# Kernel optimization log

Hardware: AMD Instinct MI355X
Metric: run time of the kernel (lower is better)

The kernel has to match this reference:

```python
import jax, jax.numpy as jnp
import numpy as np

N_NODES = 100000
N_EDGES = 800000
N_GRAPHS = 64
D_IN = 128
D_HID = 128
D_OUT = 128
N_VARS = 8


def setup_inputs() -> dict:
    key = jax.random.key(0)
    ks = jax.random.split(key, 12)
    s = 1.0 / np.sqrt(D_IN)
    inp = {
        "features": jax.random.normal(ks[0], (N_NODES, D_IN), jnp.float32),
        "src": jax.random.randint(ks[1], (N_EDGES,), 0, N_NODES, jnp.int32),
        "dst": jax.random.randint(ks[2], (N_EDGES,), 0, N_NODES, jnp.int32),
        "graph_id": jnp.sort(jax.random.randint(ks[3], (N_NODES,), 0, N_GRAPHS, jnp.int32)),
        # GINConv MLP params (Linear + ReLU per layer)
        "W1": jax.random.normal(ks[4], (D_IN, D_HID), jnp.float32) * s,
        "b1": jnp.zeros((D_HID,), jnp.float32),
        "W2": jax.random.normal(ks[5], (D_HID, D_HID), jnp.float32) * s,
        "b2": jnp.zeros((D_HID,), jnp.float32),
        "W3": jax.random.normal(ks[6], (D_HID, D_OUT), jnp.float32) * s,
        "b3": jnp.zeros((D_OUT,), jnp.float32),
        # final prediction head
        "Wp": jax.random.normal(ks[7], (D_OUT, N_VARS), jnp.float32) * s,
        "bp": jnp.zeros((N_VARS,), jnp.float32),
    }
    return inp


def reference(features, src, dst, graph_id, W1, b1, W2, b2, W3, b3, Wp, bp):
    N = features.shape[0]

    def gin_layer(x, W, b):
        # DGL GINConv with eps=0: apply_func(x + sum_{j in N(i)} x_j)
        agg = jax.ops.segment_sum(x[src], dst, num_segments=N)  # [N, d]
        return jax.nn.relu((x + agg) @ W + b)

    h = gin_layer(features, W1, b1)  # dropout p=0 -> identity
    h = gin_layer(h, W2, b2)
    h = gin_layer(h, W3, b3)

    # dgl.mean_nodes: ragged per-graph mean readout
    sums = jax.ops.segment_sum(h, graph_id, num_segments=N_GRAPHS)          # [G, d]
    cnts = jax.ops.segment_sum(jnp.ones((N, 1), h.dtype), graph_id, num_segments=N_GRAPHS)
    pooled = sums / jnp.maximum(cnts, 1.0)
    return pooled @ Wp + bp  # [G, n_vars]
```

## Files before the change

### kernel.cpp

```cpp
#include <hip/hip_runtime.h>
#include <cstddef>

#define NN 100000
#define NE 800000
#define NG 64
#define DD 128
#define NV 8
#define NS 8
#define SCAN_CH 1024
#define SCAN_NB ((NN + SCAN_CH - 1) / SCAN_CH)
#define NPC 256
#define NCHUNK ((NN + NPC - 1) / NPC)

#define CVT_BLKS 6250
#define WT_BLKS 192
#define HCH 392
#define ECH ((NE + HCH - 1) / HCH)
#define RNG 12500

typedef __attribute__((ext_vector_type(8))) short bf16x8;
typedef __attribute__((ext_vector_type(4))) float f32x4;
typedef __attribute__((ext_vector_type(2))) unsigned int u32x2;

__device__ inline float lo2f(unsigned int u) {
  union { unsigned int i; float f; } x;
  x.i = u << 16;
  return x.f;
}
__device__ inline float hi2f(unsigned int u) {
  union { unsigned int i; float f; } x;
  x.i = u & 0xffff0000u;
  return x.f;
}
__device__ inline unsigned short f2b(float f) {
  union { float f; unsigned int i; } x;
  x.f = f;
  unsigned int r = x.i + 0x7fffu + ((x.i >> 16) & 1u);
  return (unsigned short)(r >> 16);
}
__device__ inline unsigned int pk(float a, float b) {
  return (unsigned int)f2b(a) | ((unsigned int)f2b(b) << 16);
}

__global__ __launch_bounds__(256) void zero_w(unsigned int* __restrict__ p, int n) {
  int i = blockIdx.x * blockDim.x + threadIdx.x;
  if (i < n) p[i] = 0u;
}

__global__ __launch_bounds__(256) void prep(const float* __restrict__ feat,
                                            const float* __restrict__ W1,
                                            const float* __restrict__ W2,
                                            const float* __restrict__ W3,
                                            const int* __restrict__ dst,
                                            unsigned short* __restrict__ xs,
                                            unsigned short* __restrict__ Wt,
                                            int* __restrict__ deg) {
  int b = blockIdx.x;
  if (b < CVT_BLKS) {
    int tid = b * 256 + threadIdx.x;
    int n = tid >> 4, part = tid & 15;
    const float* p = feat + (size_t)n * DD + part * 8;
    float4 v0 = *(const float4*)p;
    float4 v1 = *(const float4*)(p + 4);
    unsigned int u0 = pk(v0.x, v0.y), u1 = pk(v0.z, v0.w);
    unsigned int u2 = pk(v1.x, v1.y), u3 = pk(v1.z, v1.w);
    int slice = part >> 1, half = part & 1;
    *(uint4*)((char*)xs + ((size_t)slice * NN + n) * 32 + half * 16) =
        make_uint4(u0, u1, u2, u3);
  } else if (b < CVT_BLKS + WT_BLKS) {
    int idx = (b - CVT_BLKS) * 256 + threadIdx.x;
    int w = idx >> 14, r = idx & 16383;
    const float* W = (w == 0) ? W1 : (w == 1) ? W2 : W3;
    Wt[idx] = f2b(W[(r & 127) * DD + (r >> 7)]);
  } else {
    int hb = b - CVT_BLKS - WT_BLKS;
    int r = hb & 7, chunk = hb >> 3;
    int lo = r * RNG, hi = lo + RNG;
    int e0 = chunk * ECH;
    int e1 = e0 + ECH;
    if (e1 > NE) e1 = NE;
    for (int e = e0 + threadIdx.x; e < e1; e += 256) {
      int d = dst[e];
      if (d >= lo && d < hi) atomicAdd(&deg[d], 1);
    }
  }
}

__global__ __launch_bounds__(256) void scan1(const int* __restrict__ deg,
                                             int* __restrict__ excl,
                                             int* __restrict__ bsum) {
  __shared__ int ts[256];
  int base = blockIdx.x * SCAN_CH;
  int t = threadIdx.x;
  int v[4];
  int s = 0;
#pragma unroll
  for (int i = 0; i < 4; i++) {
    int idx = base + t * 4 + i;
    v[i] = (idx < NN) ? deg[idx] : 0;
    s += v[i];
  }
  ts[t] = s;
  __syncthreads();
  for (int off = 1; off < 256; off <<= 1) {
    int val = (t >= off) ? ts[t - off] : 0;
    __syncthreads();
    ts[t] += val;
    __syncthreads();
  }
  if (t == 255) bsum[blockIdx.x] = ts[255];
  int run = ts[t] - s;
#pragma unroll
  for (int i = 0; i < 4; i++) {
    int idx = base + t * 4 + i;
    if (idx < NN) excl[idx] = run;
    run += v[i];
  }
}

__global__ __launch_bounds__(128) void scan2(int* __restrict__ bsum, int nb) {
  __shared__ int sh[128];
  int t = threadIdx.x;
  int v = (t < nb) ? bsum[t] : 0;
  sh[t] = v;
  __syncthreads();
  for (int off = 1; off < 128; off <<= 1) {
    int u = (t >= off) ? sh[t - off] : 0;
    __syncthreads();
    sh[t] += u;
    __syncthreads();
  }
  if (t < nb) bsum[t] = sh[t] - v;
}

__global__ __launch_bounds__(256) void scan3(int* __restrict__ rowp,
                                             const int* __restrict__ bsum,
                                             int* __restrict__ cursor) {
  int i = blockIdx.x * blockDim.x + threadIdx.x;
  if (i < NN) {
    int v = rowp[i] + bsum[i / SCAN_CH];
    rowp[i] = v;
    cursor[i] = v;
  }
  if (i == 0) rowp[NN] = NE;
}

__global__ __launch_bounds__(256) void fill_csr(const int* __restrict__ src,
                                                const int* __restrict__ dst,
                                                int* __restrict__ cursor,
                                                int* __restrict__ csrb) {
  int r = blockIdx.x & 7, chunk = blockIdx.x >> 3;
  int lo = r * RNG, hi = lo + RNG;
  int e0 = chunk * ECH;
  int e1 = e0 + ECH;
  if (e1 > NE) e1 = NE;
  for (int e = e0 + threadIdx.x; e < e1; e += 256) {
    int d = dst[e];
    if (d >= lo && d < hi) {
      int pos = atomicAdd(&cursor[d], 1);
      csrb[pos] = src[e] << 5;
    }
  }
}

__global__ __launch_bounds__(256) void gather_slice(const unsigned short* __restrict__ xs,
                                                    const int* __restrict__ csrb,
                                                    const int* __restrict__ rowp,
                                                    unsigned short* __restrict__ aggs) {
  const int s = blockIdx.x & 7;
  const int chunk = blockIdx.x >> 3;
  const char* __restrict__ xsl = (const char*)xs + (size_t)s * NN * 32;
  char* __restrict__ asl = (char*)aggs + (size_t)s * NN * 32;
  const int li = threadIdx.x & 3;
  const int grp = threadIdx.x >> 2;
  const int node0 = chunk * NPC;
  int node1 = node0 + NPC;
  if (node1 > NN) node1 = NN;
  const int lo8 = li * 8;
  for (int n = node0 + grp; n < node1; n += 64) {
    int beg = rowp[n], end = rowp[n + 1];
    u32x2 sv = *(const u32x2*)(xsl + (size_t)n * 32 + lo8);
    float a0 = lo2f(sv.x), a1 = hi2f(sv.x), a2 = lo2f(sv.y), a3 = hi2f(sv.y);
    float c0 = 0.f, c1 = 0.f, c2 = 0.f, c3 = 0.f;
    int e = beg;
    int off = (beg < end) ? csrb[(beg + li < end) ? beg + li : end - 1] : 0;
    for (; e + 4 <= end; e += 4) {
      int ne = e + 4;
      int off_next = 0;
      if (ne < end) off_next = csrb[(ne + li < end) ? ne + li : end - 1];
      int o0 = __shfl(off, 0, 4);
      int o1 = __shfl(off, 1, 4);
      int o2 = __shfl(off, 2, 4);
      int o3 = __shfl(off, 3, 4);
      u32x2 v0 = *(const u32x2*)(xsl + (unsigned int)o0 + lo8);
      u32x2 v1 = *(const u32x2*)(xsl + (unsigned int)o1 + lo8);
      u32x2 v2 = *(const u32x2*)(xsl + (unsigned int)o2 + lo8);
      u32x2 v3 = *(const u32x2*)(xsl + (unsigned int)o3 + lo8);
      a0 += lo2f(v0.x); a1 += hi2f(v0.x); a2 += lo2f(v0.y); a3 += hi2f(v0.y);
      c0 += lo2f(v1.x); c1 += hi2f(v1.x); c2 += lo2f(v1.y); c3 += hi2f(v1.y);
      a0 += lo2f(v2.x); a1 += hi2f(v2.x); a2 += lo2f(v2.y); a3 += hi2f(v2.y);
      c0 += lo2f(v3.x); c1 += hi2f(v3.x); c2 += lo2f(v3.y); c3 += hi2f(v3.y);
      off = off_next;
    }
    if (e < end) {
      int rem = end - e;
      for (int j = 0; j < rem; j++) {
        int oj = __shfl(off, j, 4);
        u32x2 v = *(const u32x2*)(xsl + (unsigned int)oj + lo8);
        a0 += lo2f(v.x); a1 += hi2f(v.x); a2 += lo2f(v.y); a3 += hi2f(v.y);
      }
    }
    u32x2 o;
    o.x = pk(a0 + c0, a1 + c1);
    o.y = pk(a2 + c2, a3 + c3);
    *(u32x2*)(asl + (size_t)n * 32 + lo8) = o;
  }
}

template <int POOL>
__global__ __launch_bounds__(256) void gemm_mfma(const unsigned short* __restrict__ A,
                                                 const unsigned short* __restrict__ Wt,
                                                 const float* __restrict__ bias,
                                                 unsigned short* __restrict__ H,
                                                 const int* __restrict__ gid,
                                                 float* __restrict__ sums,
                                                 float* __restrict__ cnts) {
  __shared__ uint4 a_sh4[1024];
  __shared__ uint4 w_sh4[2048];
  __shared__ int gsh[64];
  char* a_sh = (char*)a_sh4;
  char* w_sh = (char*)w_sh4;
  const int t = threadIdx.x;
  const int block_row = blockIdx.x * 64;

  if (POOL) {
    if (t < 64) gsh[t] = (block_row + t < NN) ? gid[block_row + t] : -1;
  }

#pragma unroll
  for (int p = 0; p < 8; p++) {
    int lin = p * 4096 + t * 16;
    int row = lin >> 8, inner = lin & 255;
    uint4 v = *(const uint4*)((const char*)Wt + lin);
    *(uint4*)(w_sh + row * 256 + (inner ^ ((row & 7) << 4))) = v;
  }
#pragma unroll
  for (int p = 0; p < 4; p++) {
    int lin = p * 4096 + t * 16;
    int row = lin >> 8, inner = lin & 255;
    int grow = block_row + row;
    uint4 v = make_uint4(0u, 0u, 0u, 0u);
    if (grow < NN) {
      int slice = inner >> 5, half = (inner >> 4) & 1;
      v = *(const uint4*)((const char*)A + ((size_t)slice * NN + grow) * 32 + half * 16);
    }
    *(uint4*)(a_sh + row * 256 + (inner ^ ((row & 7) << 4))) = v;
  }
  __syncthreads();

  const int wid = t >> 6, lane = t & 63;
  const int rowbase = wid * 16;
  const int lr = lane & 15, lk = lane >> 4;

  f32x4 acc[8];
#pragma unroll
  for (int i = 0; i < 8; i++) acc[i] = (f32x4){0.f, 0.f, 0.f, 0.f};

#pragma unroll
  for (int c = 0; c < 4; c++) {
    int arow = rowbase + lr;
    bf16x8 af = *(const bf16x8*)(a_sh + arow * 256 + ((c * 64 + lk * 16) ^ ((arow & 7) << 4)));
#pragma unroll
    for (int nt = 0; nt < 8; nt++) {
      int bcol = nt * 16 + lr;
      bf16x8 bf = *(const bf16x8*)(w_sh + bcol * 256 + ((c * 64 + lk * 16) ^ ((bcol & 7) << 4)));
      acc[nt] = __builtin_amdgcn_mfma_f32_16x16x32_bf16(af, bf, acc[nt], 0, 0, 0);
    }
  }
  __syncthreads();

  float* osh = (float*)w_sh;
#pragma unroll
  for (int nt = 0; nt < 8; nt++) {
    int col = nt * 16 + lr;
    float bv = bias[col];
#pragma unroll
    for (int r = 0; r < 4; r++) {
      int row = rowbase + lk * 4 + r;
      osh[row * 128 + col] = fmaxf(acc[nt][r] + bv, 0.f);
    }
  }
  __syncthreads();

  if (POOL == 0) {
#pragma unroll
    for (int i = 0; i < 8; i++) {
      int fidx = i * 1024 + t * 4;
      float4 v = *(const float4*)(osh + fidx);
      int row = fidx >> 7, col = fidx & 127;
      int grow = block_row + row;
      if (grow < NN) {
        int slice = col >> 4, w = col & 15;
        ushort4 o;
        o.x = f2b(v.x);
        o.y = f2b(v.y);
        o.z = f2b(v.z);
        o.w = f2b(v.w);
        *(ushort4*)(H + ((size_t)slice * NN + grow) * 16 + w) = o;
      }
    }
  } else {
    if (t < 128) {
      int f = t;
      float acc2 = 0.f;
      int cnt = 0;
      int cur = gsh[0];
      for (int r = 0; r < 64; r++) {
        int g = gsh[r];
        if (g < 0) break;
        if (g != cur) {
          unsafeAtomicAdd(&sums[cur * DD + f], acc2);
          if (f == 0) unsafeAtomicAdd(&cnts[cur], (float)cnt);
          acc2 = 0.f;
          cnt = 0;
          cur = g;
        }
        acc2 += osh[r * 128 + f];
        cnt++;
      }
      if (cur >= 0 && cnt > 0) {
        unsafeAtomicAdd(&sums[cur * DD + f], acc2);
        if (f == 0) unsafeAtomicAdd(&cnts[cur], (float)cnt);
      }
    }
  }
}

__global__ __launch_bounds__(512) void head(const float* __restrict__ sums,
                                            const float* __restrict__ cnts,
                                            const float* __restrict__ Wp,
                                            const float* __restrict__ bp,
                                            float* __restrict__ out) {
  int t = threadIdx.x;
  int g = t >> 3;
  int v = t & 7;
  float cnt = cnts[g];
  if (cnt < 1.f) cnt = 1.f;
  float acc = 0.f;
  for (int d = 0; d < DD; d++) acc += sums[g * DD + d] * Wp[d * NV + v];
  out[t] = acc / cnt + bp[v];
}

extern "C" void kernel_launch(void* const* d_in, const int* in_sizes, int n_in,
                              void* d_out, int out_size, void* d_ws, size_t ws_size,
                              hipStream_t stream) {
  const float* feat = (const float*)d_in[0];
  const int* src = (const int*)d_in[1];
  const int* dst = (const int*)d_in[2];
  const int* gid = (const int*)d_in[3];
  const float* W1 = (const float*)d_in[4];
  const float* b1 = (const float*)d_in[5];
  const float* W2 = (const float*)d_in[6];
  const float* b2 = (const float*)d_in[7];
  const float* W3 = (const float*)d_in[8];
  const float* b3 = (const float*)d_in[9];
  const float* Wp = (const float*)d_in[10];
  const float* bp = (const float*)d_in[11];
  float* out = (float*)d_out;

  char* ws = (char*)d_ws;
  const size_t matb = (size_t)NN * DD;
  unsigned short* xs0 = (unsigned short*)ws;
  unsigned short* hs = xs0 + matb;
  unsigned short* aggs = hs + matb;
  unsigned short* wtb = aggs + matb;
  float* sums = (float*)(wtb + 3 * DD * DD);
  float* cnts = sums + NG * DD;
  int* deg = (int*)(cnts + NG);
  int* rowp = deg + NN;
  int* cursor = rowp + NN + 1;
  int* bsum = cursor + NN;
  int* csrb = bsum + 128;

  const int nzero = NG * DD + NG + NN;
  zero_w<<<(nzero + 255) / 256, 256, 0, stream>>>((unsigned int*)sums, nzero);

  prep<<<CVT_BLKS + WT_BLKS + 8 * HCH, 256, 0, stream>>>(feat, W1, W2, W3, dst, xs0, wtb, deg);

  scan1<<<SCAN_NB, 256, 0, stream>>>(deg, rowp, bsum);
  scan2<<<1, 128, 0, stream>>>(bsum, SCAN_NB);
  scan3<<<(NN + 255) / 256, 256, 0, stream>>>(rowp, bsum, cursor);
  fill_csr<<<8 * HCH, 256, 0, stream>>>(src, dst, cursor, csrb);

  const int ggrid = NCHUNK * NS;
  const int mgrid = (NN + 63) / 64;
  gather_slice<<<ggrid, 256, 0, stream>>>(xs0, csrb, rowp, aggs);
  gemm_mfma<0><<<mgrid, 256, 0, stream>>>(aggs, wtb, b1, hs, nullptr, nullptr, nullptr);
  gather_slice<<<ggrid, 256, 0, stream>>>(hs, csrb, rowp, aggs);
  gemm_mfma<0><<<mgrid, 256, 0, stream>>>(aggs, wtb + DD * DD, b2, xs0, nullptr, nullptr, nullptr);
  gather_slice<<<ggrid, 256, 0, stream>>>(xs0, csrb, rowp, aggs);
  gemm_mfma<1><<<mgrid, 256, 0, stream>>>(aggs, wtb + 2 * DD * DD, b3, nullptr, gid, sums, cnts);

  head<<<1, 512, 0, stream>>>(sums, cnts, Wp, bp, out);
}
```

Measured before the change: 307.0 us.

## Stage CSR indices in LDS for gather, simplify degree histogram, use memset

The gather kernel now loads each chunk's row pointers and up to MAXE CSR offsets into shared memory, then reads neighbour indices from LDS with an 8-way unrolled loop. This replaces the per-lane global index loads and shuffles. The degree histogram no longer makes 8 range-filtered passes over dst; it does one atomic per edge. The zeroing kernel is replaced by hipMemsetAsync. Together these trade extra LDS use and lower occupancy, plus more atomic contention, for fewer redundant global loads.

After: 322.8 us. 5.2% more time.

```diff
diff --git a/kernel.cpp b/kernel.cpp
--- a/kernel.cpp
+++ b/kernel.cpp
@@ -11,9 +11,11 @@
 #define SCAN_NB ((NN + SCAN_CH - 1) / SCAN_CH)
 #define NPC 256
 #define NCHUNK ((NN + NPC - 1) / NPC)
+#define MAXE 3072
 
 #define CVT_BLKS 6250
 #define WT_BLKS 192
+#define HIST_BLKS 3125
 #define HCH 392
 #define ECH ((NE + HCH - 1) / HCH)
 #define RNG 12500
@@ -40,11 +42,6 @@
 }
 __device__ inline unsigned int pk(float a, float b) {
   return (unsigned int)f2b(a) | ((unsigned int)f2b(b) << 16);
-}
-
-__global__ __launch_bounds__(256) void zero_w(unsigned int* __restrict__ p, int n) {
-  int i = blockIdx.x * blockDim.x + threadIdx.x;
-  if (i < n) p[i] = 0u;
 }
 
 __global__ __launch_bounds__(256) void prep(const float* __restrict__ feat,
@@ -73,16 +70,8 @@
     const float* W = (w == 0) ? W1 : (w == 1) ? W2 : W3;
     Wt[idx] = f2b(W[(r & 127) * DD + (r >> 7)]);
   } else {
-    int hb = b - CVT_BLKS - WT_BLKS;
-    int r = hb & 7, chunk = hb >> 3;
-    int lo = r * RNG, hi = lo + RNG;
-    int e0 = chunk * ECH;
-    int e1 = e0 + ECH;
-    if (e1 > NE) e1 = NE;
-    for (int e = e0 + threadIdx.x; e < e1; e += 256) {
-      int d = dst[e];
-      if (d >= lo && d < hi) atomicAdd(&deg[d], 1);
-    }
+    int e = (b - CVT_BLKS - WT_BLKS) * 256 + threadIdx.x;
+    if (e < NE) atomicAdd(&deg[dst[e]], 1);
   }
 }
 
@@ -167,46 +156,79 @@
                                                     const int* __restrict__ csrb,
                                                     const int* __restrict__ rowp,
                                                     unsigned short* __restrict__ aggs) {
+  __shared__ int csr_sh[MAXE];
+  __shared__ int rowp_sh[NPC + 1];
   const int s = blockIdx.x & 7;
   const int chunk = blockIdx.x >> 3;
   const char* __restrict__ xsl = (const char*)xs + (size_t)s * NN * 32;
   char* __restrict__ asl = (char*)aggs + (size_t)s * NN * 32;
-  const int li = threadIdx.x & 3;
-  const int grp = threadIdx.x >> 2;
+  const int t = threadIdx.x;
   const int node0 = chunk * NPC;
   int node1 = node0 + NPC;
   if (node1 > NN) node1 = NN;
+  const int nlocal = node1 - node0;
+
+  const int ebeg = rowp[node0];
+  const int eend = rowp[node1];
+  for (int i = t; i <= nlocal; i += 256) rowp_sh[i] = rowp[node0 + i] - ebeg;
+  const int ecount = eend - ebeg;
+  const int staged = (ecount < MAXE) ? ecount : MAXE;
+  for (int i = t; i < staged; i += 256)
+    csr_sh[i] = __builtin_nontemporal_load(&csrb[ebeg + i]);
+  __syncthreads();
+
+  const int li = t & 3;
+  const int grp = t >> 2;
   const int lo8 = li * 8;
+
   for (int n = node0 + grp; n < node1; n += 64) {
-    int beg = rowp[n], end = rowp[n + 1];
+    int rbeg = rowp_sh[n - node0];
+    int rend = rowp_sh[n - node0 + 1];
     u32x2 sv = *(const u32x2*)(xsl + (size_t)n * 32 + lo8);
     float a0 = lo2f(sv.x), a1 = hi2f(sv.x), a2 = lo2f(sv.y), a3 = hi2f(sv.y);
     float c0 = 0.f, c1 = 0.f, c2 = 0.f, c3 = 0.f;
-    int e = beg;
-    int off = (beg < end) ? csrb[(beg + li < end) ? beg + li : end - 1] : 0;
-    for (; e + 4 <= end; e += 4) {
-      int ne = e + 4;
-      int off_next = 0;
-      if (ne < end) off_next = csrb[(ne + li < end) ? ne + li : end - 1];
-      int o0 = __shfl(off, 0, 4);
-      int o1 = __shfl(off, 1, 4);
-      int o2 = __shfl(off, 2, 4);
-      int o3 = __shfl(off, 3, 4);
-      u32x2 v0 = *(const u32x2*)(xsl + (unsigned int)o0 + lo8);
-      u32x2 v1 = *(const u32x2*)(xsl + (unsigned int)o1 + lo8);
-      u32x2 v2 = *(const u32x2*)(xsl + (unsigned int)o2 + lo8);
-      u32x2 v3 = *(const u32x2*)(xsl + (unsigned int)o3 + lo8);
-      a0 += lo2f(v0.x); a1 += hi2f(v0.x); a2 += lo2f(v0.y); a3 += hi2f(v0.y);
-      c0 += lo2f(v1.x); c1 += hi2f(v1.x); c2 += lo2f(v1.y); c3 += hi2f(v1.y);
-      a0 += lo2f(v2.x); a1 += hi2f(v2.x); a2 += lo2f(v2.y); a3 += hi2f(v2.y);
-      c0 += lo2f(v3.x); c1 += hi2f(v3.x); c2 += lo2f(v3.y); c3 += hi2f(v3.y);
-      off = off_next;
-    }
-    if (e < end) {
-      int rem = end - e;
-      for (int j = 0; j < rem; j++) {
-        int oj = __shfl(off, j, 4);
-        u32x2 v = *(const u32x2*)(xsl + (unsigned int)oj + lo8);
+    if (rend <= staged) {
+      int e = rbeg;
+      for (; e + 8 <= rend; e += 8) {
+        int o0 = csr_sh[e], o1 = csr_sh[e + 1], o2 = csr_sh[e + 2], o3 = csr_sh[e + 3];
+        int o4 = csr_sh[e + 4], o5 = csr_sh[e + 5], o6 = csr_sh[e + 6], o7 = csr_sh[e + 7];
+        u32x2 v0 = *(const u32x2*)(xsl + (unsigned int)o0 + lo8);
+        u32x2 v1 = *(const u32x2*)(xsl + (unsigned int)o1 + lo8);
+        u32x2 v2 = *(const u32x2*)(xsl + (unsigned int)o2 + lo8);
+        u32x2 v3 = *(const u32x2*)(xsl + (unsigned int)o3 + lo8);
+        u32x2 v4 = *(const u32x2*)(xsl + (unsigned int)o4 + lo8);
+        u32x2 v5 = *(const u32x2*)(xsl + (unsigned int)o5 + lo8);
+        u32x2 v6 = *(const u32x2*)(xsl + (unsigned int)o6 + lo8);
+        u32x2 v7 = *(const u32x2*)(xsl + (unsigned int)o7 + lo8);
+        a0 += lo2f(v0.x); a1 += hi2f(v0.x); a2 += lo2f(v0.y); a3 += hi2f(v0.y);
+        c0 += lo2f(v1.x); c1 += hi2f(v1.x); c2 += lo2f(v1.y); c3 += hi2f(v1.y);
+        a0 += lo2f(v2.x); a1 += hi2f(v2.x); a2 += lo2f(v2.y); a3 += hi2f(v2.y);
+        c0 += lo2f(v3.x); c1 += hi2f(v3.x); c2 += lo2f(v3.y); c3 += hi2f(v3.y);
+        a0 += lo2f(v4.x); a1 += hi2f(v4.x); a2 += lo2f(v4.y); a3 += hi2f(v4.y);
+        c0 += lo2f(v5.x); c1 += hi2f(v5.x); c2 += lo2f(v5.y); c3 += hi2f(v5.y);
+        a0 += lo2f(v6.x); a1 += hi2f(v6.x); a2 += lo2f(v6.y); a3 += hi2f(v6.y);
+        c0 += lo2f(v7.x); c1 += hi2f(v7.x); c2 += lo2f(v7.y); c3 += hi2f(v7.y);
+      }
+      for (; e + 4 <= rend; e += 4) {
+        int o0 = csr_sh[e], o1 = csr_sh[e + 1], o2 = csr_sh[e + 2], o3 = csr_sh[e + 3];
+        u32x2 v0 = *(const u32x2*)(xsl + (unsigned int)o0 + lo8);
+        u32x2 v1 = *(const u32x2*)(xsl + (unsigned int)o1 + lo8);
+        u32x2 v2 = *(const u32x2*)(xsl + (unsigned int)o2 + lo8);
+        u32x2 v3 = *(const u32x2*)(xsl + (unsigned int)o3 + lo8);
+        a0 += lo2f(v0.x); a1 += hi2f(v0.x); a2 += lo2f(v0.y); a3 += hi2f(v0.y);
+        c0 += lo2f(v1.x); c1 += hi2f(v1.x); c2 += lo2f(v1.y); c3 += hi2f(v1.y);
+        a0 += lo2f(v2.x); a1 += hi2f(v2.x); a2 += lo2f(v2.y); a3 += hi2f(v2.y);
+        c0 += lo2f(v3.x); c1 += hi2f(v3.x); c2 += lo2f(v3.y); c3 += hi2f(v3.y);
+      }
+      for (; e < rend; e++) {
+        int o = csr_sh[e];
+        u32x2 v = *(const u32x2*)(xsl + (unsigned int)o + lo8);
+        a0 += lo2f(v.x); a1 += hi2f(v.x); a2 += lo2f(v.y); a3 += hi2f(v.y);
+      }
+    } else {
+      for (int e = rbeg; e < rend; e++) {
+        int o = csrb[ebeg + e];
+        u32x2 v = *(const u32x2*)(xsl + (unsigned int)o + lo8);
         a0 += lo2f(v.x); a1 += hi2f(v.x); a2 += lo2f(v.y); a3 += hi2f(v.y);
       }
     }
@@ -383,9 +405,9 @@
   int* csrb = bsum + 128;
 
   const int nzero = NG * DD + NG + NN;
-  zero_w<<<(nzero + 255) / 256, 256, 0, stream>>>((unsigned int*)sums, nzero);
-
-  prep<<<CVT_BLKS + WT_BLKS + 8 * HCH, 256, 0, stream>>>(feat, W1, W2, W3, dst, xs0, wtb, deg);
+  hipMemsetAsync(sums, 0, (size_t)nzero * 4, stream);
+
+  prep<<<CVT_BLKS + WT_BLKS + HIST_BLKS, 256, 0, stream>>>(feat, W1, W2, W3, dst, xs0, wtb, deg);
 
   scan1<<<SCAN_NB, 256, 0, stream>>>(deg, rowp, bsum);
   scan2<<<1, 128, 0, stream>>>(bsum, SCAN_NB);
```

## Process gather nodes in degree-sorted order to balance per-group work

Applied to the files above, without the earlier changes.

Adds a degree histogram, bin scan and counting-sort scatter that build a node order grouped by in-degree. Gather kernels then walk nodes in this order, so threads handling neighbouring nodes see similar edge counts and divergence shrinks. The degree count becomes a plain per-edge atomic instead of the range-partitioned loop, and zeroing moves to hipMemsetAsync. In exchange it adds three small kernels and an indirection load, and gathered rows and output writes become less sequential.

New measurement: 387.5 us. +26.2%, slower.

```diff
diff --git a/kernel.cpp b/kernel.cpp
--- a/kernel.cpp
+++ b/kernel.cpp
@@ -14,6 +14,7 @@
 
 #define CVT_BLKS 6250
 #define WT_BLKS 192
+#define HIST_BLKS 3125
 #define HCH 392
 #define ECH ((NE + HCH - 1) / HCH)
 #define RNG 12500
@@ -40,11 +41,6 @@
 }
 __device__ inline unsigned int pk(float a, float b) {
   return (unsigned int)f2b(a) | ((unsigned int)f2b(b) << 16);
-}
-
-__global__ __launch_bounds__(256) void zero_w(unsigned int* __restrict__ p, int n) {
-  int i = blockIdx.x * blockDim.x + threadIdx.x;
-  if (i < n) p[i] = 0u;
 }
 
 __global__ __launch_bounds__(256) void prep(const float* __restrict__ feat,
@@ -73,17 +69,58 @@
     const float* W = (w == 0) ? W1 : (w == 1) ? W2 : W3;
     Wt[idx] = f2b(W[(r & 127) * DD + (r >> 7)]);
   } else {
-    int hb = b - CVT_BLKS - WT_BLKS;
-    int r = hb & 7, chunk = hb >> 3;
-    int lo = r * RNG, hi = lo + RNG;
-    int e0 = chunk * ECH;
-    int e1 = e0 + ECH;
-    if (e1 > NE) e1 = NE;
-    for (int e = e0 + threadIdx.x; e < e1; e += 256) {
-      int d = dst[e];
-      if (d >= lo && d < hi) atomicAdd(&deg[d], 1);
-    }
-  }
+    int e = (b - CVT_BLKS - WT_BLKS) * 256 + threadIdx.x;
+    if (e < NE) atomicAdd(&deg[dst[e]], 1);
+  }
+}
+
+__global__ __launch_bounds__(256) void deg_hist(const int* __restrict__ deg,
+                                                int* __restrict__ dbin) {
+  __shared__ int h[64];
+  if (threadIdx.x < 64) h[threadIdx.x] = 0;
+  __syncthreads();
+  int i = blockIdx.x * 256 + threadIdx.x;
+  if (i < NN) atomicAdd(&h[min(deg[i], 63)], 1);
+  __syncthreads();
+  if (threadIdx.x < 64) {
+    int c = h[threadIdx.x];
+    if (c > 0) atomicAdd(&dbin[threadIdx.x], c);
+  }
+}
+
+__global__ __launch_bounds__(64) void bin_scan(const int* __restrict__ dbin,
+                                               int* __restrict__ bcur) {
+  int t = threadIdx.x;
+  int d = dbin[t];
+  int v = d;
+  for (int off = 1; off < 64; off <<= 1) {
+    int u = __shfl_up(v, off);
+    if (t >= off) v += u;
+  }
+  bcur[t] = v - d;
+}
+
+__global__ __launch_bounds__(256) void deg_scatter(const int* __restrict__ deg,
+                                                   int* __restrict__ bcur,
+                                                   int* __restrict__ order) {
+  __shared__ int lh[64];
+  __shared__ int base[64];
+  if (threadIdx.x < 64) lh[threadIdx.x] = 0;
+  __syncthreads();
+  int i = blockIdx.x * 256 + threadIdx.x;
+  int d = 0, lpos = 0;
+  bool valid = (i < NN);
+  if (valid) {
+    d = min(deg[i], 63);
+    lpos = atomicAdd(&lh[d], 1);
+  }
+  __syncthreads();
+  if (threadIdx.x < 64) {
+    int c = lh[threadIdx.x];
+    base[threadIdx.x] = (c > 0) ? atomicAdd(&bcur[threadIdx.x], c) : 0;
+  }
+  __syncthreads();
+  if (valid) order[base[d] + lpos] = i;
 }
 
 __global__ __launch_bounds__(256) void scan1(const int* __restrict__ deg,
@@ -166,6 +203,7 @@
 __global__ __launch_bounds__(256) void gather_slice(const unsigned short* __restrict__ xs,
                                                     const int* __restrict__ csrb,
                                                     const int* __restrict__ rowp,
+                                                    const int* __restrict__ order,
                                                     unsigned short* __restrict__ aggs) {
   const int s = blockIdx.x & 7;
   const int chunk = blockIdx.x >> 3;
@@ -173,11 +211,12 @@
   char* __restrict__ asl = (char*)aggs + (size_t)s * NN * 32;
   const int li = threadIdx.x & 3;
   const int grp = threadIdx.x >> 2;
-  const int node0 = chunk * NPC;
-  int node1 = node0 + NPC;
-  if (node1 > NN) node1 = NN;
+  const int pos0 = chunk * NPC;
+  int pos1 = pos0 + NPC;
+  if (pos1 > NN) pos1 = NN;
   const int lo8 = li * 8;
-  for (int n = node0 + grp; n < node1; n += 64) {
+  for (int p = pos0 + grp; p < pos1; p += 64) {
+    int n = order[p];
     int beg = rowp[n], end = rowp[n + 1];
     u32x2 sv = *(const u32x2*)(xsl + (size_t)n * 32 + lo8);
     float a0 = lo2f(sv.x), a1 = hi2f(sv.x), a2 = lo2f(sv.y), a3 = hi2f(sv.y);
@@ -381,11 +420,19 @@
   int* cursor = rowp + NN + 1;
   int* bsum = cursor + NN;
   int* csrb = bsum + 128;
+  int* order = csrb + NE;
+  int* dbin = order + NN;
+  int* bcur = dbin + 64;
 
   const int nzero = NG * DD + NG + NN;
-  zero_w<<<(nzero + 255) / 256, 256, 0, stream>>>((unsigned int*)sums, nzero);
-
-  prep<<<CVT_BLKS + WT_BLKS + 8 * HCH, 256, 0, stream>>>(feat, W1, W2, W3, dst, xs0, wtb, deg);
+  hipMemsetAsync(sums, 0, (size_t)nzero * 4, stream);
+  hipMemsetAsync(dbin, 0, 64 * 4, stream);
+
+  prep<<<CVT_BLKS + WT_BLKS + HIST_BLKS, 256, 0, stream>>>(feat, W1, W2, W3, dst, xs0, wtb, deg);
+
+  deg_hist<<<(NN + 255) / 256, 256, 0, stream>>>(deg, dbin);
+  bin_scan<<<1, 64, 0, stream>>>(dbin, bcur);
+  deg_scatter<<<(NN + 255) / 256, 256, 0, stream>>>(deg, bcur, order);
 
   scan1<<<SCAN_NB, 256, 0, stream>>>(deg, rowp, bsum);
   scan2<<<1, 128, 0, stream>>>(bsum, SCAN_NB);
@@ -394,11 +441,11 @@
 
   const int ggrid = NCHUNK * NS;
   const int mgrid = (NN + 63) / 64;
-  gather_slice<<<ggrid, 256, 0, stream>>>(xs0, csrb, rowp, aggs);
+  gather_slice<<<ggrid, 256, 0, stream>>>(xs0, csrb, rowp, order, aggs);
   gemm_mfma<0><<<mgrid, 256, 0, stream>>>(aggs, wtb, b1, hs, nullptr, nullptr, nullptr);
-  gather_slice<<<ggrid, 256, 0, stream>>>(hs, csrb, rowp, aggs);
+  gather_slice<<<ggrid, 256, 0, stream>>>(hs, csrb, rowp, order, aggs);
   gemm_mfma<0><<<mgrid, 256, 0, stream>>>(aggs, wtb + DD * DD, b2, xs0, nullptr, nullptr, nullptr);
-  gather_slice<<<ggrid, 256, 0, stream>>>(xs0, csrb, rowp, aggs);
+  gather_slice<<<ggrid, 256, 0, stream>>>(xs0, csrb, rowp, order, aggs);
   gemm_mfma<1><<<mgrid, 256, 0, stream>>>(aggs, wtb + 2 * DD * DD, b3, nullptr, gid, sums, cnts);
 
   head<<<1, 512, 0, stream>>>(sums, cnts, Wp, bp, out);
```
